# Kernel optimization log

Measured on AMD Instinct MI355X. Metric: run time of the kernel, lower is better.

The kernel has to match this reference:

```python
import jax, jax.numpy as jnp
import numpy as np
import math

B, S, H, N = 1, 4096, 1024, 16
HN = H // N  # 64

def setup_inputs() -> dict:
    key = jax.random.key(0)
    k1, k2, k3 = jax.random.split(key, 3)
    hidden_states = jax.random.normal(k1, (B, S, H), dtype=jnp.float32)
    # lower-triangular causal mask, float {0,1}, broadcastable to [b,np,s,s]
    ltor_mask = jnp.tril(jnp.ones((1, 1, S, S), dtype=jnp.float32))
    w_qkv = jax.random.normal(k2, (3 * H, H), dtype=jnp.float32) * 0.02
    b_qkv = jnp.zeros((3 * H,), dtype=jnp.float32)
    w_dense = jax.random.normal(k3, (H, H), dtype=jnp.float32) * 0.02
    b_dense = jnp.zeros((H,), dtype=jnp.float32)
    return {"hidden_states": hidden_states, "ltor_mask": ltor_mask,
            "w_qkv": w_qkv, "b_qkv": b_qkv,
            "w_dense": w_dense, "b_dense": b_dense}

def reference(hidden_states, ltor_mask, w_qkv, b_qkv, w_dense, b_dense):
    b, s, h = hidden_states.shape
    # fused QKV projection: [b,s,3h]
    mixed = jnp.einsum('bsh,oh->bso', hidden_states, w_qkv) + b_qkv
    q, k, v = jnp.split(mixed, 3, axis=-1)
    # [b,s,h] -> [b,n,s,hn]
    def heads(t):
        return t.reshape(b, s, N, HN).transpose(0, 2, 1, 3)
    q, k, v = heads(q), heads(k), heads(v)
    # raw scores [b,n,s,s]
    scores = jnp.einsum('bnqd,bnkd->bnqk', q, k) / math.sqrt(HN)
    # multiplicative mask plus -10000 additive for masked positions
    scores = scores * ltor_mask - 10000.0 * (1.0 - ltor_mask)
    probs = jax.nn.softmax(scores, axis=-1)
    # attention dropout prob = 0.0 -> identity
    ctx = jnp.einsum('bnqk,bnkd->bnqd', probs, v)
    ctx = ctx.transpose(0, 2, 1, 3).reshape(b, s, h)
    out = jnp.einsum('bsh,oh->bso', ctx, w_dense) + b_dense
    # output dropout prob = 0.0 -> identity
    return out
```

## Files before the change

kernel.cpp:

```cpp
#include <hip/hip_runtime.h>
#include <hip/hip_bf16.h>

static constexpr int SEQ  = 4096;
static constexpr int HID  = 1024;
static constexpr int NHEAD = 16;
static constexpr int HDIM  = 64;
static constexpr int H3   = 3072;

typedef __attribute__((ext_vector_type(8))) __bf16 bf16x8;
typedef __attribute__((ext_vector_type(4))) float  f32x4;

__device__ __forceinline__ float bf2f(unsigned short u) {
    union { unsigned int u; float f; } v; v.u = ((unsigned int)u) << 16; return v.f;
}
__device__ __forceinline__ unsigned short f2bf(float f) {
    union { float f; unsigned int u; } v; v.f = f;
    unsigned int r = v.u + 0x7fffu + ((v.u >> 16) & 1u);
    return (unsigned short)(r >> 16);
}
__device__ __forceinline__ void gl_lds16(const unsigned short* g, unsigned short* l) {
    __builtin_amdgcn_global_load_lds(
        (const __attribute__((address_space(1))) void*)g,
        (__attribute__((address_space(3))) void*)l, 16, 0, 0);
}

struct Conv5 { const float* src[5]; unsigned short* dst[5]; };

__global__ __launch_bounds__(256) void convert5(Conv5 c) {
    constexpr int cnt[5]  = {4194304, 3145728, 3072, 1048576, 1024};
    constexpr int boff[5] = {0, 2048, 3584, 3586, 4098};
    const int b = blockIdx.x;
    int t = 0, rel = b;
#pragma unroll
    for (int k = 1; k < 5; ++k) if (b >= boff[k]) { t = k; rel = b - boff[k]; }
    const int base = rel * 2048 + threadIdx.x * 8;
    if (base >= cnt[t]) return;
    const float* s = c.src[t] + base;
    const float4 a = ((const float4*)s)[0];
    const float4 b2 = ((const float4*)s)[1];
    union { unsigned short v[8]; uint4 q; } u;
    u.v[0] = f2bf(a.x); u.v[1] = f2bf(a.y); u.v[2] = f2bf(a.z); u.v[3] = f2bf(a.w);
    u.v[4] = f2bf(b2.x); u.v[5] = f2bf(b2.y); u.v[6] = f2bf(b2.z); u.v[7] = f2bf(b2.w);
    *(uint4*)(c.dst[t] + base) = u.q;
}

template <int BM, int BN, typename OutT>
__global__ __launch_bounds__(256) void gemm_bt(
    const unsigned short* __restrict__ A, const unsigned short* __restrict__ B,
    const unsigned short* __restrict__ bias, OutT* __restrict__ C,
    int M, int N, int K)
{
    constexpr int MI = BM / 32;
    constexpr int NI = BN / 32;
    const int tid  = threadIdx.x;
    const int wave = tid >> 6, lane = tid & 63;
    const int quad = lane >> 4, c16 = lane & 15;
    const int m0 = blockIdx.y * BM, n0 = blockIdx.x * BN;
    const int wr = wave >> 1, wc = wave & 1;

    __shared__ __align__(16) unsigned short sA[BM * 32];
    __shared__ __align__(16) unsigned short sB[BN * 32];

    f32x4 acc[MI][NI];
#pragma unroll
    for (int i = 0; i < MI; ++i)
#pragma unroll
        for (int j = 0; j < NI; ++j) acc[i][j] = {0.f, 0.f, 0.f, 0.f};

    const int sr = lane >> 2;
    const int sc = (((lane & 3) ^ ((lane >> 2) & 3))) * 8;

    for (int k0 = 0; k0 < K; k0 += 32) {
#pragma unroll
        for (int cc = 0; cc < BM / 64; ++cc) {
            const int rbase = cc * 64 + wave * 16;
            gl_lds16(A + (size_t)(m0 + rbase + sr) * K + k0 + sc, &sA[rbase * 32]);
        }
#pragma unroll
        for (int cc = 0; cc < BN / 64; ++cc) {
            const int rbase = cc * 64 + wave * 16;
            gl_lds16(B + (size_t)(n0 + rbase + sr) * K + k0 + sc, &sB[rbase * 32]);
        }
        __syncthreads();

        bf16x8 af[MI], bfr[NI];
#pragma unroll
        for (int i = 0; i < MI; ++i) {
            const int ra = wr * (BM / 2) + i * 16 + c16;
            af[i] = *(const bf16x8*)&sA[ra * 32 + (quad ^ (ra & 3)) * 8];
        }
#pragma unroll
        for (int j = 0; j < NI; ++j) {
            const int rb = wc * (BN / 2) + j * 16 + c16;
            bfr[j] = *(const bf16x8*)&sB[rb * 32 + (quad ^ (rb & 3)) * 8];
        }
#pragma unroll
        for (int i = 0; i < MI; ++i)
#pragma unroll
            for (int j = 0; j < NI; ++j)
                acc[i][j] = __builtin_amdgcn_mfma_f32_16x16x32_bf16(af[i], bfr[j], acc[i][j], 0, 0, 0);
        __syncthreads();
    }

#pragma unroll
    for (int j = 0; j < NI; ++j) {
        const int col = n0 + wc * (BN / 2) + j * 16 + c16;
        const float bv = bf2f(bias[col]);
#pragma unroll
        for (int i = 0; i < MI; ++i) {
#pragma unroll
            for (int r = 0; r < 4; ++r) {
                const int row = m0 + wr * (BM / 2) + i * 16 + quad * 4 + r;
                const float v = acc[i][j][r] + bv;
                if constexpr (sizeof(OutT) == 2) C[(size_t)row * N + col] = (OutT)f2bf(v);
                else                             C[(size_t)row * N + col] = (OutT)v;
            }
        }
    }
}

__global__ __launch_bounds__(256) void transpose_v(
    const unsigned short* __restrict__ qkv, unsigned short* __restrict__ vt)
{
    const int n  = blockIdx.x >> 6;
    const int s0 = (blockIdx.x & 63) << 6;
    const int t  = threadIdx.x;
    __shared__ __align__(16) unsigned short tile[64][72];

#pragma unroll
    for (int p = 0; p < 2; ++p) {
        const int si = p * 32 + (t >> 3);
        const int d0 = (t & 7) * 8;
        const uint4 v = *(const uint4*)(qkv + (size_t)(s0 + si) * H3 + 2 * HID + n * HDIM + d0);
        *(uint4*)&tile[si][d0] = v;
    }
    __syncthreads();

    const int d    = t >> 2;
    const int soff = (t & 3) << 4;
    union { unsigned short s[16]; uint2 q2[4]; } buf;
#pragma unroll
    for (int i = 0; i < 16; ++i) buf.s[i] = tile[soff + i][d];
    const int k32 = soff & 32;
    const int tb4 = (soff & 16) >> 2;
    unsigned short* dst = vt + (size_t)(n * HDIM + d) * SEQ + s0 + k32 + tb4;
#pragma unroll
    for (int b = 0; b < 4; ++b)
        *(uint2*)(dst + b * 8) = buf.q2[b];
}

__global__ __launch_bounds__(256) void attn_causal(
    const unsigned short* __restrict__ qkv, const unsigned short* __restrict__ vt,
    unsigned short* __restrict__ ctx)
{
    const int bx = blockIdx.x;
    const int n  = bx & 15;
    const int z  = bx >> 4;
    const int mz = (z & 15) | ((z >> 1) & 16);
    const int qb = (z & 16) ? (63 - mz) : mz;
    const int tid  = threadIdx.x;
    const int wave = tid >> 6, lane = tid & 63;
    const int quad = lane >> 4, c16 = lane & 15;

    __shared__ __align__(16) unsigned short smem[2 * 64 * 64];
    unsigned short* smem_k = smem;
    unsigned short* smem_v = smem + 64 * 64;

    const int qrow0 = qb * 64 + wave * 16;

    const float QS = 0.125f * 1.44269504f;
    bf16x8 qf[2];
#pragma unroll
    for (int kq = 0; kq < 2; ++kq) {
        bf16x8 q = *(const bf16x8*)(qkv + (size_t)(qrow0 + c16) * H3 + n * HDIM + kq * 32 + quad * 8);
#pragma unroll
        for (int j = 0; j < 8; ++j) q[j] = (__bf16)((float)q[j] * QS);
        qf[kq] = q;
    }

    f32x4 o[4];
#pragma unroll
    for (int dt = 0; dt < 4; ++dt) o[dt] = {0.f, 0.f, 0.f, 0.f};
    float l_i = 0.f;

    const int srow8 = lane >> 3;
    const int scol8 = ((lane & 7) ^ (lane >> 3)) * 8;
    const int q_g   = qrow0 + c16;

    const int nkb = qb + 1;
    for (int kb = 0; kb < nkb; ++kb) {
        const int kv0 = kb * 64;
#pragma unroll
        for (int cc = 0; cc < 2; ++cc) {
            const int rbase = wave * 16 + cc * 8;
            gl_lds16(qkv + (size_t)(kv0 + rbase + srow8) * H3 + HID + n * HDIM + scol8,
                     &smem_k[rbase * 64]);
            gl_lds16(vt + (size_t)(n * HDIM + rbase + srow8) * SEQ + kv0 + scol8,
                     &smem_v[rbase * 64]);
        }
        __syncthreads();

        f32x4 s[4];
#pragma unroll
        for (int mt = 0; mt < 4; ++mt) s[mt] = {0.f, 0.f, 0.f, 0.f};
#pragma unroll
        for (int mt = 0; mt < 4; ++mt) {
            const int row = mt * 16 + c16;
            const bf16x8 kf0 = *(const bf16x8*)&smem_k[row * 64 + ((quad)     ^ (row & 7)) * 8];
            const bf16x8 kf1 = *(const bf16x8*)&smem_k[row * 64 + ((4 + quad) ^ (row & 7)) * 8];
            s[mt] = __builtin_amdgcn_mfma_f32_16x16x32_bf16(kf0, qf[0], s[mt], 0, 0, 0);
            s[mt] = __builtin_amdgcn_mfma_f32_16x16x32_bf16(kf1, qf[1], s[mt], 0, 0, 0);
        }

        if (kb == qb) {
#pragma unroll
            for (int mt = 0; mt < 4; ++mt)
#pragma unroll
                for (int r = 0; r < 4; ++r) {
                    const int kv = kv0 + mt * 16 + quad * 4 + r;
                    if (kv > q_g) s[mt][r] = -30000.0f;
                }
        }

        float rs = 0.f;
#pragma unroll
        for (int mt = 0; mt < 4; ++mt)
#pragma unroll
            for (int r = 0; r < 4; ++r) {
                const float p = __builtin_amdgcn_exp2f(s[mt][r]);
                s[mt][r] = p;
                rs += p;
            }
        l_i += rs;

        bf16x8 pf[2];
#pragma unroll
        for (int kc = 0; kc < 2; ++kc) {
            union { __bf16 b[8]; bf16x8 v; } pp;
#pragma unroll
            for (int r = 0; r < 4; ++r) {
                pp.b[r]     = (__bf16)s[2 * kc][r];
                pp.b[4 + r] = (__bf16)s[2 * kc + 1][r];
            }
            pf[kc] = pp.v;
        }

#pragma unroll
        for (int kc = 0; kc < 2; ++kc) {
#pragma unroll
            for (int dt = 0; dt < 4; ++dt) {
                const int row = dt * 16 + c16;
                const int c8 = (kc * 4 + quad) ^ (row & 7);
                const bf16x8 vf = *(const bf16x8*)&smem_v[row * 64 + c8 * 8];
                o[dt] = __builtin_amdgcn_mfma_f32_16x16x32_bf16(vf, pf[kc], o[dt], 0, 0, 0);
            }
        }
        __syncthreads();
    }

    l_i += __shfl_xor(l_i, 16);
    l_i += __shfl_xor(l_i, 32);
    const float inv = 1.0f / l_i;

    unsigned short* sc_ = smem + wave * 1152;
#pragma unroll
    for (int dt = 0; dt < 4; ++dt) {
        union { unsigned short u[4]; uint2 q2; } w;
#pragma unroll
        for (int r = 0; r < 4; ++r) w.u[r] = f2bf(o[dt][r] * inv);
        *(uint2*)&sc_[c16 * 72 + dt * 16 + quad * 4] = w.q2;
    }
    const int qr = lane >> 2;
    const int xc = (lane & 3) * 16;
    union { unsigned short us[16]; uint4 q4[2]; } ob;
    *(uint4*)&ob.us[0] = *(const uint4*)&sc_[qr * 72 + xc];
    *(uint4*)&ob.us[8] = *(const uint4*)&sc_[qr * 72 + xc + 8];
    unsigned short* dst = ctx + (size_t)(qrow0 + qr) * HID + n * HDIM + xc;
    *(uint4*)dst       = ob.q4[0];
    *(uint4*)(dst + 8) = ob.q4[1];
}

extern "C" void kernel_launch(void* const* d_in, const int* in_sizes, int n_in,
                              void* d_out, int out_size, void* d_ws, size_t ws_size,
                              hipStream_t stream)
{
    unsigned short* base = (unsigned short*)d_ws;

    unsigned short* hs_c = base;
    unsigned short* wq_c = hs_c + 4194304;
    unsigned short* bq_c = wq_c + 3145728;
    unsigned short* wd_c = bq_c + 3072;
    unsigned short* bd_c = wd_c + 1048576;
    unsigned short* qkv  = bd_c + 1024;
    unsigned short* vt   = qkv + (size_t)SEQ * H3;
    unsigned short* ctx  = hs_c;

    Conv5 c;
    c.src[0] = (const float*)d_in[0]; c.src[1] = (const float*)d_in[2];
    c.src[2] = (const float*)d_in[3]; c.src[3] = (const float*)d_in[4];
    c.src[4] = (const float*)d_in[5];
    c.dst[0] = hs_c; c.dst[1] = wq_c; c.dst[2] = bq_c; c.dst[3] = wd_c; c.dst[4] = bd_c;
    hipLaunchKernelGGL(convert5, dim3(4099), dim3(256), 0, stream, c);

    hipLaunchKernelGGL((gemm_bt<128, 128, unsigned short>), dim3(H3 / 128, SEQ / 128), dim3(256), 0, stream,
                       hs_c, wq_c, bq_c, qkv, SEQ, H3, HID);
    hipLaunchKernelGGL(transpose_v, dim3(NHEAD * (SEQ / 64)), dim3(256), 0, stream, qkv, vt);
    hipLaunchKernelGGL(attn_causal, dim3(NHEAD * (SEQ / 64)), dim3(256), 0, stream, qkv, vt, ctx);
    hipLaunchKernelGGL((gemm_bt<64, 128, float>), dim3(HID / 128, SEQ / 64), dim3(256), 0, stream,
                       ctx, wd_c, bd_c, (float*)d_out, SEQ, HID, HID);
}
```

Baseline: 250.7 us.

## Enlarge attention query tile to 128 rows and parametrize GEMM K-tile

The attention kernel now handles 128 query rows per block, with each wave computing 32 rows as two 16-row subtiles. Each K/V tile loaded into LDS is therefore reused across twice as many queries, halving the K/V global traffic and the per-tile barriers. Fully masked subtiles are skipped. The GEMM gains a BK template parameter, and the output projection uses BK=64 to cut loop iterations and syncs. The cost is fewer attention blocks (512), which lowers parallelism and load balance, plus higher register pressure per wave.

```diff
diff --git a/kernel.cpp b/kernel.cpp
--- a/kernel.cpp
+++ b/kernel.cpp
@@ -44,22 +44,27 @@
     *(uint4*)(c.dst[t] + base) = u.q;
 }
 
-template <int BM, int BN, typename OutT>
+template <int BM, int BN, int BK, typename OutT>
 __global__ __launch_bounds__(256) void gemm_bt(
     const unsigned short* __restrict__ A, const unsigned short* __restrict__ B,
     const unsigned short* __restrict__ bias, OutT* __restrict__ C,
     int M, int N, int K)
 {
-    constexpr int MI = BM / 32;
-    constexpr int NI = BN / 32;
+    constexpr int MI  = BM / 32;
+    constexpr int NI  = BN / 32;
+    constexpr int KC  = BK / 32;
+    constexpr int CB  = BK / 8;
+    constexpr int LSH = (BK == 32) ? 2 : 3;
+    constexpr int RPC = 64 >> LSH;
+
     const int tid  = threadIdx.x;
     const int wave = tid >> 6, lane = tid & 63;
     const int quad = lane >> 4, c16 = lane & 15;
     const int m0 = blockIdx.y * BM, n0 = blockIdx.x * BN;
     const int wr = wave >> 1, wc = wave & 1;
 
-    __shared__ __align__(16) unsigned short sA[BM * 32];
-    __shared__ __align__(16) unsigned short sB[BN * 32];
+    __shared__ __align__(16) unsigned short sA[BM * BK];
+    __shared__ __align__(16) unsigned short sB[BN * BK];
 
     f32x4 acc[MI][NI];
 #pragma unroll
@@ -67,38 +72,44 @@
 #pragma unroll
         for (int j = 0; j < NI; ++j) acc[i][j] = {0.f, 0.f, 0.f, 0.f};
 
-    const int sr = lane >> 2;
-    const int sc = (((lane & 3) ^ ((lane >> 2) & 3))) * 8;
-
-    for (int k0 = 0; k0 < K; k0 += 32) {
-#pragma unroll
-        for (int cc = 0; cc < BM / 64; ++cc) {
-            const int rbase = cc * 64 + wave * 16;
-            gl_lds16(A + (size_t)(m0 + rbase + sr) * K + k0 + sc, &sA[rbase * 32]);
-        }
-#pragma unroll
-        for (int cc = 0; cc < BN / 64; ++cc) {
-            const int rbase = cc * 64 + wave * 16;
-            gl_lds16(B + (size_t)(n0 + rbase + sr) * K + k0 + sc, &sB[rbase * 32]);
+    const int sr = lane >> LSH;
+    const int sc = ((lane & (CB - 1)) ^ (sr & (CB - 1))) * 8;
+
+    for (int k0 = 0; k0 < K; k0 += BK) {
+#pragma unroll
+        for (int cc = 0; cc < BM / RPC / 4; ++cc) {
+            const int rbase = cc * (4 * RPC) + wave * RPC;
+            gl_lds16(A + (size_t)(m0 + rbase + sr) * K + k0 + sc, &sA[rbase * BK]);
+        }
+#pragma unroll
+        for (int cc = 0; cc < BN / RPC / 4; ++cc) {
+            const int rbase = cc * (4 * RPC) + wave * RPC;
+            gl_lds16(B + (size_t)(n0 + rbase + sr) * K + k0 + sc, &sB[rbase * BK]);
         }
         __syncthreads();
 
-        bf16x8 af[MI], bfr[NI];
+        bf16x8 af[MI][KC], bfr[NI][KC];
 #pragma unroll
         for (int i = 0; i < MI; ++i) {
             const int ra = wr * (BM / 2) + i * 16 + c16;
-            af[i] = *(const bf16x8*)&sA[ra * 32 + (quad ^ (ra & 3)) * 8];
+#pragma unroll
+            for (int kc = 0; kc < KC; ++kc)
+                af[i][kc] = *(const bf16x8*)&sA[ra * BK + (((kc * 4 + quad) ^ ra) & (CB - 1)) * 8];
         }
 #pragma unroll
         for (int j = 0; j < NI; ++j) {
             const int rb = wc * (BN / 2) + j * 16 + c16;
-            bfr[j] = *(const bf16x8*)&sB[rb * 32 + (quad ^ (rb & 3)) * 8];
+#pragma unroll
+            for (int kc = 0; kc < KC; ++kc)
+                bfr[j][kc] = *(const bf16x8*)&sB[rb * BK + (((kc * 4 + quad) ^ rb) & (CB - 1)) * 8];
         }
 #pragma unroll
         for (int i = 0; i < MI; ++i)
 #pragma unroll
             for (int j = 0; j < NI; ++j)
-                acc[i][j] = __builtin_amdgcn_mfma_f32_16x16x32_bf16(af[i], bfr[j], acc[i][j], 0, 0, 0);
+#pragma unroll
+                for (int kc = 0; kc < KC; ++kc)
+                    acc[i][j] = __builtin_amdgcn_mfma_f32_16x16x32_bf16(af[i][kc], bfr[j][kc], acc[i][j], 0, 0, 0);
         __syncthreads();
     }
 
@@ -156,38 +167,40 @@
     const int bx = blockIdx.x;
     const int n  = bx & 15;
     const int z  = bx >> 4;
-    const int mz = (z & 15) | ((z >> 1) & 16);
-    const int qb = (z & 16) ? (63 - mz) : mz;
+    const int qb = (z < 16) ? z : 47 - z;
     const int tid  = threadIdx.x;
     const int wave = tid >> 6, lane = tid & 63;
     const int quad = lane >> 4, c16 = lane & 15;
 
-    __shared__ __align__(16) unsigned short smem[2 * 64 * 64];
+    __shared__ __align__(16) unsigned short smem[9216];
     unsigned short* smem_k = smem;
-    unsigned short* smem_v = smem + 64 * 64;
-
-    const int qrow0 = qb * 64 + wave * 16;
+    unsigned short* smem_v = smem + 4096;
+
+    const int qrow0 = qb * 128 + wave * 32;
 
     const float QS = 0.125f * 1.44269504f;
-    bf16x8 qf[2];
-#pragma unroll
-    for (int kq = 0; kq < 2; ++kq) {
-        bf16x8 q = *(const bf16x8*)(qkv + (size_t)(qrow0 + c16) * H3 + n * HDIM + kq * 32 + quad * 8);
-#pragma unroll
-        for (int j = 0; j < 8; ++j) q[j] = (__bf16)((float)q[j] * QS);
-        qf[kq] = q;
-    }
-
-    f32x4 o[4];
-#pragma unroll
-    for (int dt = 0; dt < 4; ++dt) o[dt] = {0.f, 0.f, 0.f, 0.f};
-    float l_i = 0.f;
+    bf16x8 qf[2][2];
+#pragma unroll
+    for (int wq = 0; wq < 2; ++wq)
+#pragma unroll
+        for (int kc = 0; kc < 2; ++kc) {
+            bf16x8 q = *(const bf16x8*)(qkv + (size_t)(qrow0 + wq * 16 + c16) * H3 + n * HDIM + kc * 32 + quad * 8);
+#pragma unroll
+            for (int j = 0; j < 8; ++j) q[j] = (__bf16)((float)q[j] * QS);
+            qf[wq][kc] = q;
+        }
+
+    f32x4 o[2][4];
+#pragma unroll
+    for (int wq = 0; wq < 2; ++wq)
+#pragma unroll
+        for (int dt = 0; dt < 4; ++dt) o[wq][dt] = {0.f, 0.f, 0.f, 0.f};
+    float l_i[2] = {0.f, 0.f};
 
     const int srow8 = lane >> 3;
     const int scol8 = ((lane & 7) ^ (lane >> 3)) * 8;
-    const int q_g   = qrow0 + c16;
-
-    const int nkb = qb + 1;
+
+    const int nkb = 2 * qb + 2;
     for (int kb = 0; kb < nkb; ++kb) {
         const int kv0 = kb * 64;
 #pragma unroll
@@ -200,84 +213,102 @@
         }
         __syncthreads();
 
-        f32x4 s[4];
-#pragma unroll
-        for (int mt = 0; mt < 4; ++mt) s[mt] = {0.f, 0.f, 0.f, 0.f};
-#pragma unroll
-        for (int mt = 0; mt < 4; ++mt) {
-            const int row = mt * 16 + c16;
-            const bf16x8 kf0 = *(const bf16x8*)&smem_k[row * 64 + ((quad)     ^ (row & 7)) * 8];
-            const bf16x8 kf1 = *(const bf16x8*)&smem_k[row * 64 + ((4 + quad) ^ (row & 7)) * 8];
-            s[mt] = __builtin_amdgcn_mfma_f32_16x16x32_bf16(kf0, qf[0], s[mt], 0, 0, 0);
-            s[mt] = __builtin_amdgcn_mfma_f32_16x16x32_bf16(kf1, qf[1], s[mt], 0, 0, 0);
-        }
-
-        if (kb == qb) {
-#pragma unroll
-            for (int mt = 0; mt < 4; ++mt)
-#pragma unroll
-                for (int r = 0; r < 4; ++r) {
-                    const int kv = kv0 + mt * 16 + quad * 4 + r;
-                    if (kv > q_g) s[mt][r] = -30000.0f;
+        if (kv0 <= qrow0 + 31) {
+            f32x4 s[2][4];
+#pragma unroll
+            for (int wq = 0; wq < 2; ++wq)
+#pragma unroll
+                for (int mt = 0; mt < 4; ++mt) s[wq][mt] = {0.f, 0.f, 0.f, 0.f};
+#pragma unroll
+            for (int mt = 0; mt < 4; ++mt) {
+                const int row = mt * 16 + c16;
+                const bf16x8 kf0 = *(const bf16x8*)&smem_k[row * 64 + ((quad)     ^ (row & 7)) * 8];
+                const bf16x8 kf1 = *(const bf16x8*)&smem_k[row * 64 + ((4 + quad) ^ (row & 7)) * 8];
+#pragma unroll
+                for (int wq = 0; wq < 2; ++wq) {
+                    s[wq][mt] = __builtin_amdgcn_mfma_f32_16x16x32_bf16(kf0, qf[wq][0], s[wq][mt], 0, 0, 0);
+                    s[wq][mt] = __builtin_amdgcn_mfma_f32_16x16x32_bf16(kf1, qf[wq][1], s[wq][mt], 0, 0, 0);
                 }
-        }
-
-        float rs = 0.f;
-#pragma unroll
-        for (int mt = 0; mt < 4; ++mt)
-#pragma unroll
-            for (int r = 0; r < 4; ++r) {
-                const float p = __builtin_amdgcn_exp2f(s[mt][r]);
-                s[mt][r] = p;
-                rs += p;
             }
-        l_i += rs;
-
-        bf16x8 pf[2];
-#pragma unroll
-        for (int kc = 0; kc < 2; ++kc) {
-            union { __bf16 b[8]; bf16x8 v; } pp;
-#pragma unroll
-            for (int r = 0; r < 4; ++r) {
-                pp.b[r]     = (__bf16)s[2 * kc][r];
-                pp.b[4 + r] = (__bf16)s[2 * kc + 1][r];
+
+#pragma unroll
+            for (int wq = 0; wq < 2; ++wq) {
+                if (kv0 + 63 > qrow0 + wq * 16) {
+                    const int q_g = qrow0 + wq * 16 + c16;
+#pragma unroll
+                    for (int mt = 0; mt < 4; ++mt)
+#pragma unroll
+                        for (int r = 0; r < 4; ++r) {
+                            const int kv = kv0 + mt * 16 + quad * 4 + r;
+                            if (kv > q_g) s[wq][mt][r] = -30000.0f;
+                        }
+                }
+                float rs = 0.f;
+#pragma unroll
+                for (int mt = 0; mt < 4; ++mt)
+#pragma unroll
+                    for (int r = 0; r < 4; ++r) {
+                        const float p = __builtin_amdgcn_exp2f(s[wq][mt][r]);
+                        s[wq][mt][r] = p;
+                        rs += p;
+                    }
+                l_i[wq] += rs;
             }
-            pf[kc] = pp.v;
-        }
-
-#pragma unroll
-        for (int kc = 0; kc < 2; ++kc) {
-#pragma unroll
-            for (int dt = 0; dt < 4; ++dt) {
-                const int row = dt * 16 + c16;
-                const int c8 = (kc * 4 + quad) ^ (row & 7);
-                const bf16x8 vf = *(const bf16x8*)&smem_v[row * 64 + c8 * 8];
-                o[dt] = __builtin_amdgcn_mfma_f32_16x16x32_bf16(vf, pf[kc], o[dt], 0, 0, 0);
+
+            bf16x8 pf[2][2];
+#pragma unroll
+            for (int wq = 0; wq < 2; ++wq)
+#pragma unroll
+                for (int kc = 0; kc < 2; ++kc) {
+                    union { __bf16 b[8]; bf16x8 v; } pp;
+#pragma unroll
+                    for (int r = 0; r < 4; ++r) {
+                        pp.b[r]     = (__bf16)s[wq][2 * kc][r];
+                        pp.b[4 + r] = (__bf16)s[wq][2 * kc + 1][r];
+                    }
+                    pf[wq][kc] = pp.v;
+                }
+
+#pragma unroll
+            for (int kc = 0; kc < 2; ++kc) {
+#pragma unroll
+                for (int dt = 0; dt < 4; ++dt) {
+                    const int row = dt * 16 + c16;
+                    const int c8 = (kc * 4 + quad) ^ (row & 7);
+                    const bf16x8 vf = *(const bf16x8*)&smem_v[row * 64 + c8 * 8];
+#pragma unroll
+                    for (int wq = 0; wq < 2; ++wq)
+                        o[wq][dt] = __builtin_amdgcn_mfma_f32_16x16x32_bf16(vf, pf[wq][kc], o[wq][dt], 0, 0, 0);
+                }
             }
         }
         __syncthreads();
     }
 
-    l_i += __shfl_xor(l_i, 16);
-    l_i += __shfl_xor(l_i, 32);
-    const float inv = 1.0f / l_i;
-
-    unsigned short* sc_ = smem + wave * 1152;
-#pragma unroll
-    for (int dt = 0; dt < 4; ++dt) {
-        union { unsigned short u[4]; uint2 q2; } w;
-#pragma unroll
-        for (int r = 0; r < 4; ++r) w.u[r] = f2bf(o[dt][r] * inv);
-        *(uint2*)&sc_[c16 * 72 + dt * 16 + quad * 4] = w.q2;
-    }
-    const int qr = lane >> 2;
-    const int xc = (lane & 3) * 16;
-    union { unsigned short us[16]; uint4 q4[2]; } ob;
-    *(uint4*)&ob.us[0] = *(const uint4*)&sc_[qr * 72 + xc];
-    *(uint4*)&ob.us[8] = *(const uint4*)&sc_[qr * 72 + xc + 8];
+    float inv[2];
+#pragma unroll
+    for (int wq = 0; wq < 2; ++wq) {
+        float l = l_i[wq];
+        l += __shfl_xor(l, 16);
+        l += __shfl_xor(l, 32);
+        inv[wq] = 1.0f / l;
+    }
+    unsigned short* sc_ = smem + wave * 2304;
+#pragma unroll
+    for (int wq = 0; wq < 2; ++wq)
+#pragma unroll
+        for (int dt = 0; dt < 4; ++dt) {
+            union { unsigned short u[4]; uint2 q2; } w;
+#pragma unroll
+            for (int r = 0; r < 4; ++r) w.u[r] = f2bf(o[wq][dt][r] * inv[wq]);
+            *(uint2*)&sc_[(wq * 16 + c16) * 72 + dt * 16 + quad * 4] = w.q2;
+        }
+    const int qr = lane >> 1;
+    const int xc = (lane & 1) * 32;
     unsigned short* dst = ctx + (size_t)(qrow0 + qr) * HID + n * HDIM + xc;
-    *(uint4*)dst       = ob.q4[0];
-    *(uint4*)(dst + 8) = ob.q4[1];
+#pragma unroll
+    for (int i = 0; i < 4; ++i)
+        *(uint4*)(dst + i * 8) = *(const uint4*)&sc_[qr * 72 + xc + i * 8];
 }
 
 extern "C" void kernel_launch(void* const* d_in, const int* in_sizes, int n_in,
@@ -302,10 +333,10 @@
     c.dst[0] = hs_c; c.dst[1] = wq_c; c.dst[2] = bq_c; c.dst[3] = wd_c; c.dst[4] = bd_c;
     hipLaunchKernelGGL(convert5, dim3(4099), dim3(256), 0, stream, c);
 
-    hipLaunchKernelGGL((gemm_bt<128, 128, unsigned short>), dim3(H3 / 128, SEQ / 128), dim3(256), 0, stream,
+    hipLaunchKernelGGL((gemm_bt<128, 128, 32, unsigned short>), dim3(H3 / 128, SEQ / 128), dim3(256), 0, stream,
                        hs_c, wq_c, bq_c, qkv, SEQ, H3, HID);
     hipLaunchKernelGGL(transpose_v, dim3(NHEAD * (SEQ / 64)), dim3(256), 0, stream, qkv, vt);
-    hipLaunchKernelGGL(attn_causal, dim3(NHEAD * (SEQ / 64)), dim3(256), 0, stream, qkv, vt, ctx);
-    hipLaunchKernelGGL((gemm_bt<64, 128, float>), dim3(HID / 128, SEQ / 64), dim3(256), 0, stream,
+    hipLaunchKernelGGL(attn_causal, dim3(NHEAD * (SEQ / 128)), dim3(256), 0, stream, qkv, vt, ctx);
+    hipLaunchKernelGGL((gemm_bt<64, 128, 64, float>), dim3(HID / 128, SEQ / 64), dim3(256), 0, stream,
                        ctx, wd_c, bd_c, (float*)d_out, SEQ, HID, HID);
 }
```

Result: slower. 260.3 us (+3.8%).
